# Performance work log

Hardware: AMD Instinct MI355X
Metric: run time of the kernel (lower is better)

## Reference

```python
import jax, jax.numpy as jnp
import numpy as np

IN_CH, OUT_CH = 32, 32
MODES1, MODES2 = 16, 16
B, L, H, W = 8, 16, 64, 33


def setup_inputs() -> dict:
    key = jax.random.key(0)
    k = jax.random.split(key, 6)
    scale = 1.0 / (IN_CH * OUT_CH)
    wshape = (IN_CH, OUT_CH, MODES1, MODES2)
    return {
        "x_re": jax.random.normal(k[0], (B, L, IN_CH, H, W), dtype=jnp.float32),
        "x_im": jax.random.normal(k[1], (B, L, IN_CH, H, W), dtype=jnp.float32),
        "w1_re": scale * jax.random.normal(k[2], wshape, dtype=jnp.float32),
        "w1_im": scale * jax.random.normal(k[3], wshape, dtype=jnp.float32),
        "w2_re": scale * jax.random.normal(k[4], wshape, dtype=jnp.float32),
        "w2_im": scale * jax.random.normal(k[5], wshape, dtype=jnp.float32),
    }


def _mul2d(x, w):
    # x: [B, L, C_in, m1, m2] complex; w: [C_in, C_out, m1, m2] complex
    return jnp.einsum("blcij,coij->bloij", x, w)


def reference(x_re, x_im, w1_re, w1_im, w2_re, w2_im):
    x = jax.lax.complex(x_re, x_im)          # [B, L, C, H, W] complex64
    w1 = jax.lax.complex(w1_re, w1_im)       # [C_in, C_out, m1, m2]
    w2 = jax.lax.complex(w2_re, w2_im)
    Bx, Lx, Cx, Hx, Wx = x.shape
    m1 = min(Hx, MODES1)
    m2 = min(Wx, MODES2)

    out = jnp.zeros((Bx, Lx, OUT_CH, Hx, Wx), dtype=x.dtype)
    # low positive frequencies (top-left corner)
    out = out.at[:, :, :, :m1, :m2].set(
        _mul2d(x[:, :, :, :m1, :m2], w1[:, :, :m1, :m2]))
    # low negative frequencies along H (bottom-left corner)
    if Hx > 1 and (Hx > MODES1 or Wx > MODES2):
        out = out.at[:, :, :, -m1:, :m2].set(
            _mul2d(x[:, :, :, -m1:, :m2], w2[:, :, :m1, :m2]))
    # return complex result as trailing real/imag dim (float32)
    return jnp.stack([out.real, out.imag], axis=-1)
```

## Files before the change

kernel.cpp:

```cpp
#include <hip/hip_runtime.h>

#define HW 2112L
typedef float f32x4 __attribute__((ext_vector_type(4)));
typedef short s16x8 __attribute__((ext_vector_type(8)));

#define WT_PLANE 1048576L
#define OFF_WHR 0L
#define OFF_WLR (WT_PLANE)
#define OFF_WHI (2*WT_PLANE)
#define OFF_WLI (3*WT_PLANE)

__device__ __forceinline__ ushort f2bf(float f) {
    unsigned u = __float_as_uint(f);
    u += 0x7FFF + ((u >> 16) & 1);
    return (ushort)(u >> 16);
}
__device__ __forceinline__ void split_bf(float v, ushort& hi, ushort& lo) {
    hi = f2bf(v);
    float hf = __uint_as_float(((unsigned)hi) << 16);
    lo = f2bf(v - hf);
}

__global__ __launch_bounds__(256) void w_prep(
    const float* __restrict__ w1_re, const float* __restrict__ w1_im,
    const float* __restrict__ w2_re, const float* __restrict__ w2_im,
    char* __restrict__ ws)
{
    const int tid = threadIdx.x, bid = blockIdx.x;
    const int r = bid >> 6, i = (bid >> 2) & 15, nt = (bid >> 1) & 1, kh = bid & 1;
    const float* wre = r ? w2_re : w1_re;
    const float* wim = r ? w2_im : w1_im;
    const int col = tid >> 4, j = tid & 15, o = nt * 16 + col;
    const int modeLin = (r * 16 + i) * 16 + j;
    s16x8* phr = (s16x8*)(ws + OFF_WHR);
    s16x8* plr = (s16x8*)(ws + OFF_WLR);
    s16x8* phi = (s16x8*)(ws + OFF_WHI);
    s16x8* pli = (s16x8*)(ws + OFF_WLI);
    #pragma unroll
    for (int kk = 0; kk < 2; ++kk) {
        const int kg = kh * 2 + kk;
        s16x8 hr, lr, hi2, li2;
        #pragma unroll
        for (int e = 0; e < 8; ++e) {
            int c = kg * 8 + e;
            long src = ((long)(c * 32 + o) * 16 + i) * 16 + j;
            ushort a, b;
            split_bf(wre[src], a, b); hr[e] = (short)a; lr[e] = (short)b;
            split_bf(wim[src], a, b); hi2[e] = (short)a; li2[e] = (short)b;
        }
        long off = (long)(modeLin * 2 + nt) * 64 + kg * 16 + col;
        phr[off] = hr; plr[off] = lr; phi[off] = hi2; pli[off] = li2;
    }
}

__global__ __launch_bounds__(256) void fill_mid(float* __restrict__ out) {
    int gtid = blockIdx.x * 256 + threadIdx.x, n = 1024 * 256;
    float4* out4 = (float4*)out;
    const float4 z = make_float4(0.f, 0.f, 0.f, 0.f);
    for (int idx = gtid; idx < 4096 * 528; idx += n) {
        int plane = idx / 528;
        int k = idx - plane * 528;
        out4[(long)plane * 1056 + 264 + k] = z;
    }
}

__global__ __launch_bounds__(256, 4) void k3_compute(
    const float* __restrict__ x_re, const float* __restrict__ x_im,
    float* __restrict__ out, const char* __restrict__ ws)
{
    const int tid = threadIdx.x, bid = blockIdx.x;
    const int g = bid & 63, i = bid >> 6;
    const int r = g >> 5, bt = g & 31;
    const int h = r ? 48 + i : i;
    const int bl0 = bt * 4;
    const int modeBase = (r * 16 + i) * 16;

    __shared__ __align__(16) ushort xfr[16][4][32];
    __shared__ __align__(16) ushort xfi[16][4][32];
    __shared__ __align__(16) float2 stg[128][17];

    const int wave = tid >> 6, lane = tid & 63;
    const int m = lane & 3, ks = lane >> 4, colo = lane & 15;

    const s16x8* Bwhr = (const s16x8*)(ws + OFF_WHR);
    const s16x8* Bwlr = (const s16x8*)(ws + OFF_WLR);
    const s16x8* Bwhi = (const s16x8*)(ws + OFF_WHI);
    const s16x8* Bwli = (const s16x8*)(ws + OFF_WLI);

    const int j0 = wave * 4;
    s16x8 cBhr[2], cBlr[2], cBhi[2], cBli[2];
    {
        long b0 = ((long)(modeBase + j0) * 2 + 0) * 64 + lane;
        long b1 = ((long)(modeBase + j0) * 2 + 1) * 64 + lane;
        cBhr[0] = Bwhr[b0]; cBlr[0] = Bwlr[b0]; cBhi[0] = Bwhi[b0]; cBli[0] = Bwli[b0];
        cBhr[1] = Bwhr[b1]; cBlr[1] = Bwlr[b1]; cBhi[1] = Bwhi[b1]; cBli[1] = Bwli[b1];
    }

    #pragma unroll
    for (int p = 0; p < 2; ++p) {
        int idx = p * 256 + tid;
        int j4 = idx & 3, row = idx >> 2;
        int c = row >> 2, bl = row & 3;
        long base = ((long)((bl0 + bl) * 32 + c)) * HW + h * 33 + j4 * 4;
        float re0 = x_re[base + 0], re1 = x_re[base + 1], re2 = x_re[base + 2], re3 = x_re[base + 3];
        float im0 = x_im[base + 0], im1 = x_im[base + 1], im2 = x_im[base + 2], im3 = x_im[base + 3];
        xfr[j4 * 4 + 0][bl][c] = f2bf(re0); xfi[j4 * 4 + 0][bl][c] = f2bf(im0);
        xfr[j4 * 4 + 1][bl][c] = f2bf(re1); xfi[j4 * 4 + 1][bl][c] = f2bf(im1);
        xfr[j4 * 4 + 2][bl][c] = f2bf(re2); xfi[j4 * 4 + 2][bl][c] = f2bf(im2);
        xfr[j4 * 4 + 3][bl][c] = f2bf(re3); xfi[j4 * 4 + 3][bl][c] = f2bf(im3);
    }
    __syncthreads();

    #pragma unroll
    for (int jj = 0; jj < 4; ++jj) {
        const int j = j0 + jj;

        s16x8 nBhr[2], nBlr[2], nBhi[2], nBli[2];
        if (jj < 3) {
            long b0 = ((long)(modeBase + j + 1) * 2 + 0) * 64 + lane;
            long b1 = ((long)(modeBase + j + 1) * 2 + 1) * 64 + lane;
            nBhr[0] = Bwhr[b0]; nBlr[0] = Bwlr[b0]; nBhi[0] = Bwhi[b0]; nBli[0] = Bwli[b0];
            nBhr[1] = Bwhr[b1]; nBlr[1] = Bwlr[b1]; nBhi[1] = Bwhi[b1]; nBli[1] = Bwli[b1];
        }

        s16x8 Ahr = *(const s16x8*)&xfr[j][m][ks * 8];
        s16x8 Ahi = *(const s16x8*)&xfi[j][m][ks * 8];

        #pragma unroll
        for (int nt = 0; nt < 2; ++nt) {
            f32x4 accP = (f32x4)0.0f, accN = (f32x4)0.0f, accI = (f32x4)0.0f;
            accP = __builtin_amdgcn_mfma_f32_16x16x32_bf16(Ahr, cBhr[nt], accP, 0, 0, 0);
            accP = __builtin_amdgcn_mfma_f32_16x16x32_bf16(Ahr, cBlr[nt], accP, 0, 0, 0);
            accN = __builtin_amdgcn_mfma_f32_16x16x32_bf16(Ahi, cBhi[nt], accN, 0, 0, 0);
            accN = __builtin_amdgcn_mfma_f32_16x16x32_bf16(Ahi, cBli[nt], accN, 0, 0, 0);
            accI = __builtin_amdgcn_mfma_f32_16x16x32_bf16(Ahr, cBhi[nt], accI, 0, 0, 0);
            accI = __builtin_amdgcn_mfma_f32_16x16x32_bf16(Ahr, cBli[nt], accI, 0, 0, 0);
            accI = __builtin_amdgcn_mfma_f32_16x16x32_bf16(Ahi, cBhr[nt], accI, 0, 0, 0);
            accI = __builtin_amdgcn_mfma_f32_16x16x32_bf16(Ahi, cBlr[nt], accI, 0, 0, 0);

            if (ks == 0) {
                #pragma unroll
                for (int q = 0; q < 4; ++q)
                    stg[q * 32 + nt * 16 + colo][j] =
                        make_float2(accP[q] - accN[q], accI[q]);
            }
        }

        if (jj < 3) {
            #pragma unroll
            for (int nt = 0; nt < 2; ++nt) {
                cBhr[nt] = nBhr[nt]; cBlr[nt] = nBlr[nt];
                cBhi[nt] = nBhi[nt]; cBli[nt] = nBli[nt];
            }
        }
    }
    __syncthreads();

    float2* out2 = (float2*)out;
    #pragma unroll 2
    for (int t = 0; t < 17; ++t) {
        int idx = t * 256 + tid;
        if (idx < 128 * 33) {
            int row = idx / 33;
            int k = idx - row * 33;
            float2 v = (k < 16) ? stg[row][k] : make_float2(0.f, 0.f);
            long dst = ((long)(bl0 * 32 + row) * 64 + h) * 33 + k;
            out2[dst] = v;
        }
    }
}

extern "C" void kernel_launch(void* const* d_in, const int* in_sizes, int n_in,
                              void* d_out, int out_size, void* d_ws, size_t ws_size,
                              hipStream_t stream) {
    const float* x_re  = (const float*)d_in[0];
    const float* x_im  = (const float*)d_in[1];
    const float* w1_re = (const float*)d_in[2];
    const float* w1_im = (const float*)d_in[3];
    const float* w2_re = (const float*)d_in[4];
    const float* w2_im = (const float*)d_in[5];
    float* out = (float*)d_out;
    char* ws = (char*)d_ws;

    w_prep<<<dim3(128), dim3(256), 0, stream>>>(w1_re, w1_im, w2_re, w2_im, ws);
    fill_mid<<<dim3(1024), dim3(256), 0, stream>>>(out);
    k3_compute<<<dim3(1024), dim3(256), 0, stream>>>(x_re, x_im, out, ws);
}
```

Before: 36.49 us.

## Stage compact spectral results in workspace, then write full output contiguously

The compute kernel now writes its compact 32x16 mode results to a workspace buffer with coalesced stores, instead of scattering 33-wide rows into the output. A new placement kernel then streams the entire output as contiguous float4 stores, inserting zeros where no mode exists. This replaces the separate zero-fill kernel and removes the strided partial-row writes. In exchange, every result makes an extra round trip through workspace memory, and the placement kernel does per-element index divisions.

```diff
diff --git a/kernel.cpp b/kernel.cpp
--- a/kernel.cpp
+++ b/kernel.cpp
@@ -9,6 +9,7 @@
 #define OFF_WLR (WT_PLANE)
 #define OFF_WHI (2*WT_PLANE)
 #define OFF_WLI (3*WT_PLANE)
+#define OFF_WS2 8388608L
 
 __device__ __forceinline__ ushort f2bf(float f) {
     unsigned u = __float_as_uint(f);
@@ -53,24 +54,12 @@
     }
 }
 
-__global__ __launch_bounds__(256) void fill_mid(float* __restrict__ out) {
-    int gtid = blockIdx.x * 256 + threadIdx.x, n = 1024 * 256;
-    float4* out4 = (float4*)out;
-    const float4 z = make_float4(0.f, 0.f, 0.f, 0.f);
-    for (int idx = gtid; idx < 4096 * 528; idx += n) {
-        int plane = idx / 528;
-        int k = idx - plane * 528;
-        out4[(long)plane * 1056 + 264 + k] = z;
-    }
-}
-
-__global__ __launch_bounds__(256, 4) void k3_compute(
+__global__ __launch_bounds__(256, 4) void k_compute(
     const float* __restrict__ x_re, const float* __restrict__ x_im,
-    float* __restrict__ out, const char* __restrict__ ws)
+    char* __restrict__ ws)
 {
     const int tid = threadIdx.x, bid = blockIdx.x;
-    const int g = bid & 63, i = bid >> 6;
-    const int r = g >> 5, bt = g & 31;
+    const int r = bid >> 9, i = (bid >> 5) & 15, bt = bid & 31;
     const int h = r ? 48 + i : i;
     const int bl0 = bt * 4;
     const int modeBase = (r * 16 + i) * 16;
@@ -156,17 +145,44 @@
     }
     __syncthreads();
 
-    float2* out2 = (float2*)out;
-    #pragma unroll 2
-    for (int t = 0; t < 17; ++t) {
-        int idx = t * 256 + tid;
-        if (idx < 128 * 33) {
-            int row = idx / 33;
-            int k = idx - row * 33;
-            float2 v = (k < 16) ? stg[row][k] : make_float2(0.f, 0.f);
-            long dst = ((long)(bl0 * 32 + row) * 64 + h) * 33 + k;
-            out2[dst] = v;
-        }
+    float2* W2 = (float2*)(ws + OFF_WS2);
+    const long base = (long)bl0 * 32 * 512 + r * 256 + i * 16;
+    #pragma unroll
+    for (int p = 0; p < 8; ++p) {
+        int idx = p * 256 + tid;
+        int j = idx & 15, o = (idx >> 4) & 31, blq = idx >> 9;
+        W2[base + (long)blq * 16384 + o * 512 + j] = stg[blq * 32 + o][j];
+    }
+}
+
+__global__ __launch_bounds__(256) void k_place(
+    float* __restrict__ out, const char* __restrict__ ws)
+{
+    const int tid = threadIdx.x, bid = blockIdx.x;
+    const int bl = bid >> 2, oq = bid & 3;
+    const float2* W2 = (const float2*)(ws + OFF_WS2);
+    float4* out4 = (float4*)out;
+    const long outbase4 = ((long)bl * 32 + oq * 8) * 1056;
+    const long wbase    = ((long)bl * 32 + oq * 8) * 512;
+
+    #pragma unroll 1
+    for (int p = 0; p < 33; ++p) {
+        int idx = p * 256 + tid;
+        int ol = idx / 1056;
+        int f  = idx - ol * 1056;
+        int g0 = f * 2, g1 = g0 + 1;
+        int h0 = g0 / 33, w0 = g0 - h0 * 33;
+        int h1 = g1 / 33, w1 = g1 - h1 * 33;
+        float4 v = make_float4(0.f, 0.f, 0.f, 0.f);
+        if (w0 < 16 && (h0 < 16 || h0 >= 48)) {
+            float2 t = W2[wbase + (long)ol * 512 + (h0 < 16 ? h0 * 16 : 256 + (h0 - 48) * 16) + w0];
+            v.x = t.x; v.y = t.y;
+        }
+        if (w1 < 16 && (h1 < 16 || h1 >= 48)) {
+            float2 t = W2[wbase + (long)ol * 512 + (h1 < 16 ? h1 * 16 : 256 + (h1 - 48) * 16) + w1];
+            v.z = t.x; v.w = t.y;
+        }
+        out4[outbase4 + (long)ol * 1056 + f] = v;
     }
 }
 
@@ -183,6 +199,6 @@
     char* ws = (char*)d_ws;
 
     w_prep<<<dim3(128), dim3(256), 0, stream>>>(w1_re, w1_im, w2_re, w2_im, ws);
-    fill_mid<<<dim3(1024), dim3(256), 0, stream>>>(out);
-    k3_compute<<<dim3(1024), dim3(256), 0, stream>>>(x_re, x_im, out, ws);
-}
+    k_compute<<<dim3(1024), dim3(256), 0, stream>>>(x_re, x_im, ws);
+    k_place<<<dim3(512), dim3(256), 0, stream>>>(out, ws);
+}
```

Measured after the change: 41.07 us. +12.5%, slower.

## Merge weight prep with zero-fill and split compute blocks over mode halves

Applied to the files above, without the earlier changes.

The weight bf16-split prep and the zero-fill of the middle frequency rows are merged into one launch: 64 blocks do the prep and the remaining 1984 do the fill. The compute kernel now splits each (row, batch-tile) block into two halves along the W modes, giving 2048 smaller blocks with less shared memory and a launch-bounds occupancy hint of 5. X loads switch to 16-byte vector loads. The aim is to cut one launch, raise parallelism and occupancy, and balance the output writes, though each block now does less work and the two halves write uneven amounts of output.

```diff
diff --git a/kernel.cpp b/kernel.cpp
--- a/kernel.cpp
+++ b/kernel.cpp
@@ -21,13 +21,27 @@
     lo = f2bf(v - hf);
 }
 
-__global__ __launch_bounds__(256) void w_prep(
+__global__ __launch_bounds__(256) void k1_prep_fill(
     const float* __restrict__ w1_re, const float* __restrict__ w1_im,
     const float* __restrict__ w2_re, const float* __restrict__ w2_im,
-    char* __restrict__ ws)
+    float* __restrict__ out, char* __restrict__ ws)
 {
     const int tid = threadIdx.x, bid = blockIdx.x;
-    const int r = bid >> 6, i = (bid >> 2) & 15, nt = (bid >> 1) & 1, kh = bid & 1;
+
+    if (bid >= 64) {
+        const int fid = bid - 64;
+        int gtid = fid * 256 + tid, n = 1984 * 256;
+        float4* out4 = (float4*)out;
+        const float4 z = make_float4(0.f, 0.f, 0.f, 0.f);
+        for (int idx = gtid; idx < 4096 * 528; idx += n) {
+            int plane = idx / 528;
+            int k = idx - plane * 528;
+            out4[(long)plane * 1056 + 264 + k] = z;
+        }
+        return;
+    }
+
+    const int r = bid >> 5, i = (bid >> 1) & 15, nt = bid & 1;
     const float* wre = r ? w2_re : w1_re;
     const float* wim = r ? w2_im : w1_im;
     const int col = tid >> 4, j = tid & 15, o = nt * 16 + col;
@@ -37,8 +51,7 @@
     s16x8* phi = (s16x8*)(ws + OFF_WHI);
     s16x8* pli = (s16x8*)(ws + OFF_WLI);
     #pragma unroll
-    for (int kk = 0; kk < 2; ++kk) {
-        const int kg = kh * 2 + kk;
+    for (int kg = 0; kg < 4; ++kg) {
         s16x8 hr, lr, hi2, li2;
         #pragma unroll
         for (int e = 0; e < 8; ++e) {
@@ -53,31 +66,19 @@
     }
 }
 
-__global__ __launch_bounds__(256) void fill_mid(float* __restrict__ out) {
-    int gtid = blockIdx.x * 256 + threadIdx.x, n = 1024 * 256;
-    float4* out4 = (float4*)out;
-    const float4 z = make_float4(0.f, 0.f, 0.f, 0.f);
-    for (int idx = gtid; idx < 4096 * 528; idx += n) {
-        int plane = idx / 528;
-        int k = idx - plane * 528;
-        out4[(long)plane * 1056 + 264 + k] = z;
-    }
-}
-
-__global__ __launch_bounds__(256, 4) void k3_compute(
+__global__ __launch_bounds__(256, 5) void k2_compute(
     const float* __restrict__ x_re, const float* __restrict__ x_im,
     float* __restrict__ out, const char* __restrict__ ws)
 {
     const int tid = threadIdx.x, bid = blockIdx.x;
-    const int g = bid & 63, i = bid >> 6;
-    const int r = g >> 5, bt = g & 31;
+    const int r = bid >> 10, i = (bid >> 6) & 15, bt = (bid >> 1) & 31, jh = bid & 1;
     const int h = r ? 48 + i : i;
     const int bl0 = bt * 4;
-    const int modeBase = (r * 16 + i) * 16;
+    const int modeBase = (r * 16 + i) * 16 + jh * 8;
 
-    __shared__ __align__(16) ushort xfr[16][4][32];
-    __shared__ __align__(16) ushort xfi[16][4][32];
-    __shared__ __align__(16) float2 stg[128][17];
+    __shared__ __align__(16) ushort xfr[8][4][32];
+    __shared__ __align__(16) ushort xfi[8][4][32];
+    __shared__ __align__(16) float2 stg[128][9];
 
     const int wave = tid >> 6, lane = tid & 63;
     const int m = lane & 3, ks = lane >> 4, colo = lane & 15;
@@ -87,44 +88,41 @@
     const s16x8* Bwhi = (const s16x8*)(ws + OFF_WHI);
     const s16x8* Bwli = (const s16x8*)(ws + OFF_WLI);
 
-    const int j0 = wave * 4;
     s16x8 cBhr[2], cBlr[2], cBhi[2], cBli[2];
     {
-        long b0 = ((long)(modeBase + j0) * 2 + 0) * 64 + lane;
-        long b1 = ((long)(modeBase + j0) * 2 + 1) * 64 + lane;
+        long b0 = ((long)(modeBase + wave * 2) * 2 + 0) * 64 + lane;
+        long b1 = ((long)(modeBase + wave * 2) * 2 + 1) * 64 + lane;
         cBhr[0] = Bwhr[b0]; cBlr[0] = Bwlr[b0]; cBhi[0] = Bwhi[b0]; cBli[0] = Bwli[b0];
         cBhr[1] = Bwhr[b1]; cBlr[1] = Bwlr[b1]; cBhi[1] = Bwhi[b1]; cBli[1] = Bwli[b1];
     }
 
-    #pragma unroll
-    for (int p = 0; p < 2; ++p) {
-        int idx = p * 256 + tid;
-        int j4 = idx & 3, row = idx >> 2;
-        int c = row >> 2, bl = row & 3;
-        long base = ((long)((bl0 + bl) * 32 + c)) * HW + h * 33 + j4 * 4;
-        float re0 = x_re[base + 0], re1 = x_re[base + 1], re2 = x_re[base + 2], re3 = x_re[base + 3];
-        float im0 = x_im[base + 0], im1 = x_im[base + 1], im2 = x_im[base + 2], im3 = x_im[base + 3];
-        xfr[j4 * 4 + 0][bl][c] = f2bf(re0); xfi[j4 * 4 + 0][bl][c] = f2bf(im0);
-        xfr[j4 * 4 + 1][bl][c] = f2bf(re1); xfi[j4 * 4 + 1][bl][c] = f2bf(im1);
-        xfr[j4 * 4 + 2][bl][c] = f2bf(re2); xfi[j4 * 4 + 2][bl][c] = f2bf(im2);
-        xfr[j4 * 4 + 3][bl][c] = f2bf(re3); xfi[j4 * 4 + 3][bl][c] = f2bf(im3);
+    {
+        int jq = tid & 1, c = (tid >> 1) & 31, bl = tid >> 6;
+        long base = ((long)((bl0 + bl) * 32 + c)) * HW + h * 33 + jh * 8 + jq * 4;
+        f32x4 vr = *(const f32x4*)&x_re[base];
+        f32x4 vi = *(const f32x4*)&x_im[base];
+        #pragma unroll
+        for (int q = 0; q < 4; ++q) {
+            xfr[jq * 4 + q][bl][c] = f2bf(vr[q]);
+            xfi[jq * 4 + q][bl][c] = f2bf(vi[q]);
+        }
     }
     __syncthreads();
 
     #pragma unroll
-    for (int jj = 0; jj < 4; ++jj) {
-        const int j = j0 + jj;
+    for (int jj = 0; jj < 2; ++jj) {
+        const int jl = wave * 2 + jj;
 
         s16x8 nBhr[2], nBlr[2], nBhi[2], nBli[2];
-        if (jj < 3) {
-            long b0 = ((long)(modeBase + j + 1) * 2 + 0) * 64 + lane;
-            long b1 = ((long)(modeBase + j + 1) * 2 + 1) * 64 + lane;
+        if (jj == 0) {
+            long b0 = ((long)(modeBase + jl + 1) * 2 + 0) * 64 + lane;
+            long b1 = ((long)(modeBase + jl + 1) * 2 + 1) * 64 + lane;
             nBhr[0] = Bwhr[b0]; nBlr[0] = Bwlr[b0]; nBhi[0] = Bwhi[b0]; nBli[0] = Bwli[b0];
             nBhr[1] = Bwhr[b1]; nBlr[1] = Bwlr[b1]; nBhi[1] = Bwhi[b1]; nBli[1] = Bwli[b1];
         }
 
-        s16x8 Ahr = *(const s16x8*)&xfr[j][m][ks * 8];
-        s16x8 Ahi = *(const s16x8*)&xfi[j][m][ks * 8];
+        s16x8 Ahr = *(const s16x8*)&xfr[jl][m][ks * 8];
+        s16x8 Ahi = *(const s16x8*)&xfi[jl][m][ks * 8];
 
         #pragma unroll
         for (int nt = 0; nt < 2; ++nt) {
@@ -141,12 +139,12 @@
             if (ks == 0) {
                 #pragma unroll
                 for (int q = 0; q < 4; ++q)
-                    stg[q * 32 + nt * 16 + colo][j] =
+                    stg[q * 32 + nt * 16 + colo][jl] =
                         make_float2(accP[q] - accN[q], accI[q]);
             }
         }
 
-        if (jj < 3) {
+        if (jj == 0) {
             #pragma unroll
             for (int nt = 0; nt < 2; ++nt) {
                 cBhr[nt] = nBhr[nt]; cBlr[nt] = nBlr[nt];
@@ -157,15 +155,25 @@
     __syncthreads();
 
     float2* out2 = (float2*)out;
-    #pragma unroll 2
-    for (int t = 0; t < 17; ++t) {
-        int idx = t * 256 + tid;
-        if (idx < 128 * 33) {
-            int row = idx / 33;
-            int k = idx - row * 33;
-            float2 v = (k < 16) ? stg[row][k] : make_float2(0.f, 0.f);
-            long dst = ((long)(bl0 * 32 + row) * 64 + h) * 33 + k;
-            out2[dst] = v;
+    if (jh == 0) {
+        #pragma unroll
+        for (int p = 0; p < 4; ++p) {
+            int idx = p * 256 + tid;
+            int row = idx >> 3, w = idx & 7;
+            long dst = ((long)(bl0 * 32 + row) * 64 + h) * 33 + w;
+            out2[dst] = stg[row][w];
+        }
+    } else {
+        #pragma unroll 2
+        for (int t = 0; t < 13; ++t) {
+            int idx = t * 256 + tid;
+            if (idx < 128 * 25) {
+                int row = idx / 25;
+                int wl = idx - row * 25;
+                float2 v = (wl < 8) ? stg[row][wl] : make_float2(0.f, 0.f);
+                long dst = ((long)(bl0 * 32 + row) * 64 + h) * 33 + 8 + wl;
+                out2[dst] = v;
+            }
         }
     }
 }
@@ -182,7 +190,7 @@
     float* out = (float*)d_out;
     char* ws = (char*)d_ws;
 
-    w_prep<<<dim3(128), dim3(256), 0, stream>>>(w1_re, w1_im, w2_re, w2_im, ws);
-    fill_mid<<<dim3(1024), dim3(256), 0, stream>>>(out);
-    k3_compute<<<dim3(1024), dim3(256), 0, stream>>>(x_re, x_im, out, ws);
+    k1_prep_fill<<<dim3(2048), dim3(256), 0, stream>>>(
+        w1_re, w1_im, w2_re, w2_im, out, ws);
+    k2_compute<<<dim3(2048), dim3(256), 0, stream>>>(x_re, x_im, out, ws);
 }
```

Result: slower. 38.98 us (+6.8%).
